# Kernel tuning notes

Measured on AMD Instinct MI355X. Metric: run time of the kernel, lower is better.

The kernel has to match this reference:

```python
import jax, jax.numpy as jnp
import numpy as np

B, T_DEC, T_ENC = 64, 128, 256
D_X, N_HIDDEN, N_FEED = 1024, 1024, 1024


def _glorot(key, shape):
    fan_in = shape[0]
    return jax.random.normal(key, shape, dtype=jnp.float32) / np.sqrt(fan_in)


def setup_inputs() -> dict:
    key = jax.random.key(0)
    ks = jax.random.split(key, 10)
    H = N_HIDDEN
    return {
        "x": jax.random.normal(ks[0], (B, T_DEC, D_X), dtype=jnp.float32),
        "o_enc": jax.random.normal(ks[1], (B, T_ENC, H), dtype=jnp.float32),
        "h_enc": jax.random.normal(ks[2], (B, H), dtype=jnp.float32),
        # input-feeding FFN: Dense(n_feed, tanh), input dim = n_hidden
        "Wfeed": _glorot(ks[3], (H, N_FEED)),
        "bfeed": jnp.zeros((N_FEED,), dtype=jnp.float32),
        # GRU (keras v2, reset_after=True): kernel [n_feed+d_x, 3H], recurrent [H, 3H]
        "Wx": _glorot(ks[4], (N_FEED + D_X, 3 * H)),
        "Wh": _glorot(ks[5], (H, 3 * H)),
        "bxi": jnp.zeros((3 * H,), dtype=jnp.float32),  # input bias
        "bhr": jnp.zeros((3 * H,), dtype=jnp.float32),  # recurrent bias (reset_after)
        # attention FFN: Dense(n_hidden, tanh), input dim = 2H (concat[value, h_dec])
        "Watt": _glorot(ks[6], (2 * H, H)),
        "batt": jnp.zeros((H,), dtype=jnp.float32),
    }


def reference(x, o_enc, h_enc, Wfeed, bfeed, Wx, Wh, bxi, bhr, Watt, batt):
    # x: [B, T_dec, d_x], o_enc: [B, T_enc, H], h_enc: [B, H]
    def step(carry, x_t):
        h, i_feed = carry  # h: [B,H] GRU state, i_feed: [B,H] previous attention output
        # input feeding FFN + concat with current token
        i_cat = jnp.concatenate([jnp.tanh(i_feed @ Wfeed + bfeed), x_t], axis=-1)
        # GRU cell (keras reset_after=True semantics)
        gx = i_cat @ Wx + bxi  # [B, 3H]
        gh = h @ Wh + bhr      # [B, 3H]
        xz, xr, xh = jnp.split(gx, 3, axis=-1)
        hz, hr, hh = jnp.split(gh, 3, axis=-1)
        z = jax.nn.sigmoid(xz + hz)
        r = jax.nn.sigmoid(xr + hr)
        hcand = jnp.tanh(xh + r * hh)
        h_new = z * h + (1.0 - z) * hcand  # [B, H]
        # Luong dot attention over encoder outputs
        scores = jnp.einsum('bh,bth->bt', h_new, o_enc)       # [B, T_enc]
        attn = jax.nn.softmax(scores, axis=-1)
        value = jnp.einsum('bt,bth->bh', attn, o_enc)         # [B, H]
        h_att = jnp.tanh(jnp.concatenate([value, h_new], axis=-1) @ Watt + batt)
        return (h_new, h_att), h_att

    i_feed0 = jnp.zeros_like(h_enc)
    x_t_major = jnp.swapaxes(x, 0, 1)  # [T_dec, B, d_x]
    _, outs = jax.lax.scan(step, (h_enc, i_feed0), x_t_major)
    return jnp.swapaxes(outs, 0, 1)  # [B, T_dec, H]
```

## Files before the change

kernel.cpp:

```cpp
#include <hip/hip_runtime.h>
#include <hip/hip_bf16.h>
#include <hip/hip_fp16.h>


#define NWG 256
#define NTHR 1024
constexpr int BB = 64, TD = 128, TE = 256, HH = 1024, H3 = 3072;
constexpr unsigned SMEM_BYTES = 155696;

typedef __attribute__((ext_vector_type(8))) __bf16 bf16x8;
typedef __attribute__((ext_vector_type(4))) float f32x4;
typedef __attribute__((ext_vector_type(4))) _Float16 f16x4;
using bf = __hip_bfloat16;
using hf = _Float16;

__device__ __forceinline__ f32x4 mfma16(bf16x8 a, bf16x8 b, f32x4 c) {
  return __builtin_amdgcn_mfma_f32_16x16x32_bf16(a, b, c, 0, 0, 0);
}

struct Args {
  const float *x, *bfeed, *bxi, *bhr, *batt;
  const hf *ohi, *olo;
  const bf *Wf0, *Wf1, *Wf2, *Wh0, *Wh1, *Wh2;
  const bf *WxF0, *WxF1, *WxF2, *WxX0, *WxX1, *WxX2, *Wa0, *Wa1, *Wa2;
  float *h_f32;
  float *gx;
  float *gh, *scores;
  bf *hs0, *hs1, *hs2, *ff0, *ff1, *ff2, *ifd0, *ifd1, *ifd2;
  bf *xt0, *xt1, *xt2, *vl0, *vl1, *vl2;
  unsigned *cnt, *cnt2, *go, *afl, *gox, *ffc, *ffx;
  float *out;
};

__device__ __forceinline__ void gbar(unsigned ep, const Args& a, int wg) {
  __syncthreads();
  if (threadIdx.x == 0) {
    __threadfence();
    unsigned* sub = a.cnt + (wg & 15) * 32;
    unsigned o = __hip_atomic_fetch_add(sub, 1u, __ATOMIC_ACQ_REL, __HIP_MEMORY_SCOPE_AGENT);
    if (o == 15) {
      __hip_atomic_store(sub, 0u, __ATOMIC_RELAXED, __HIP_MEMORY_SCOPE_AGENT);
      unsigned o2 = __hip_atomic_fetch_add(a.cnt2, 1u, __ATOMIC_ACQ_REL, __HIP_MEMORY_SCOPE_AGENT);
      if (o2 == 15) {
        __hip_atomic_store(a.cnt2, 0u, __ATOMIC_RELAXED, __HIP_MEMORY_SCOPE_AGENT);
        __hip_atomic_store(a.go, ep, __ATOMIC_RELEASE, __HIP_MEMORY_SCOPE_AGENT);
      }
    }
    if (wg < 8) {
      while (__hip_atomic_load(a.go, __ATOMIC_RELAXED, __HIP_MEMORY_SCOPE_AGENT) < ep)
        __builtin_amdgcn_s_sleep(1);
      __hip_atomic_store(a.gox + wg * 32, ep, __ATOMIC_RELEASE, __HIP_MEMORY_SCOPE_AGENT);
    } else {
      while (__hip_atomic_load(a.gox + (wg & 7) * 32, __ATOMIC_RELAXED,
                               __HIP_MEMORY_SCOPE_AGENT) < ep)
        __builtin_amdgcn_s_sleep(1);
    }
    __threadfence();
  }
  __syncthreads();
}

__device__ __forceinline__ void split3_write(bf* p0, bf* p1, bf* p2, size_t i, float v) {
  bf b0 = __float2bfloat16(v);
  float r1 = v - __bfloat162float(b0);
  bf b1 = __float2bfloat16(r1);
  float r2 = r1 - __bfloat162float(b1);
  p0[i] = b0; p1[i] = b1; p2[i] = __float2bfloat16(r2);
}

template <int K>
__device__ __forceinline__ f32x4 gemm6(const bf* A0, const bf* A1, const bf* A2,
                                       const bf* B0, const bf* B1, const bf* B2) {
  f32x4 c0 = {0.f, 0.f, 0.f, 0.f}, c1 = c0, c2 = c0, c3 = c0;
  bf16x8 a0 = *(const bf16x8*)(A0);
  bf16x8 a1 = *(const bf16x8*)(A1);
  bf16x8 a2 = *(const bf16x8*)(A2);
  bf16x8 b0 = *(const bf16x8*)(B0);
  bf16x8 b1 = *(const bf16x8*)(B1);
  bf16x8 b2 = *(const bf16x8*)(B2);
#pragma unroll
  for (int k = 0; k < K; k += 32) {
    bf16x8 na0, na1, na2, nb0, nb1, nb2;
    if (k + 32 < K) {
      na0 = *(const bf16x8*)(A0 + k + 32);
      na1 = *(const bf16x8*)(A1 + k + 32);
      na2 = *(const bf16x8*)(A2 + k + 32);
      nb0 = *(const bf16x8*)(B0 + k + 32);
      nb1 = *(const bf16x8*)(B1 + k + 32);
      nb2 = *(const bf16x8*)(B2 + k + 32);
    }
    c0 = mfma16(a0, b0, c0);
    c1 = mfma16(a0, b1, c1);
    c2 = mfma16(a1, b0, c2);
    c3 = mfma16(a1, b1, c3);
    c0 = mfma16(a0, b2, c0);
    c1 = mfma16(a2, b0, c1);
    if (k + 32 < K) {
      a0 = na0; a1 = na1; a2 = na2;
      b0 = nb0; b1 = nb1; b2 = nb2;
    }
  }
  f32x4 s;
#pragma unroll
  for (int i = 0; i < 4; ++i) s[i] = (c0[i] + c1[i]) + (c2[i] + c3[i]);
  return s;
}

__global__ __launch_bounds__(NTHR, 4) void decoder_main(Args a) {
  const int wg = blockIdx.x;
  const int tid = threadIdx.x;
  const int lane = tid & 63;
  const int wv = tid >> 6;
  const int lrow = lane & 15;
  const int lkg = lane >> 4;

  extern __shared__ char smem[];
  hf* o_hi     = (hf*)smem;
  float* s_u   = (float*)(smem + 131072);
  float* s_h   = (float*)(smem + 147456);
  float* s_sm  = (float*)(smem + 151552);
  float* s_val = (float*)(smem + 152576);
  int* s_idx   = (int*)(smem + 154624);
  int* s_wcnt  = (int*)(smem + 155648);
  float* s_red = (float*)(smem + 155664);

  const int b3 = wg & 63, q3 = wg >> 6;
  {
    const ushort* src = (const ushort*)(a.ohi + ((size_t)b3 * TE + q3 * 64) * HH);
    ushort* dst = (ushort*)o_hi;
#pragma unroll 4
    for (int i = tid; i < 16384; i += NTHR)
      ((ushort4*)dst)[i] = ((const ushort4*)src)[i];
  }

  unsigned ep = 0;

  for (int t = 0; t < TD; ++t) {
    {
      const bool isf = (wg < 64);
      const int j0 = (isf ? wg : wg - 64) * 16;
      const bf* A0 = isf ? a.ifd0 : a.hs0;
      const bf* A1 = isf ? a.ifd1 : a.hs1;
      const bf* A2 = isf ? a.ifd2 : a.hs2;
      const bf* B0 = isf ? a.Wf0 : a.Wh0;
      const bf* B1 = isf ? a.Wf1 : a.Wh1;
      const bf* B2 = isf ? a.Wf2 : a.Wh2;
      const int mt = wv >> 2, kq = wv & 3;
      const size_t aoff = (size_t)(mt * 16 + lrow) * HH + kq * 256 + lkg * 8;
      const size_t boff = (size_t)(j0 + lrow) * HH + kq * 256 + lkg * 8;
      f32x4 acc = gemm6<256>(A0 + aoff, A1 + aoff, A2 + aoff, B0 + boff, B1 + boff, B2 + boff);
#pragma unroll
      for (int r = 0; r < 4; ++r) s_u[kq * 1024 + mt * 256 + (lkg * 4 + r) * 16 + lrow] = acc[r];
      __syncthreads();
      {
        const int row = tid >> 4, c = tid & 15;
        const int emt = row >> 4, r2 = row & 15;
        const int e = emt * 256 + r2 * 16 + c;
        float v = (s_u[e] + s_u[1024 + e]) + (s_u[2048 + e] + s_u[3072 + e]);
        const int col = j0 + c;
        if (isf) {
          float f = tanhf(v + a.bfeed[col]);
          split3_write(a.ff0, a.ff1, a.ff2, (size_t)row * HH + col, f);
        } else {
          a.gh[(size_t)row * H3 + col] = v + a.bhr[col];
        }
      }
      __syncthreads();
      if (isf && tid == 0) {
        __threadfence();
        __hip_atomic_fetch_add(a.ffc, 1u, __ATOMIC_ACQ_REL, __HIP_MEMORY_SCOPE_AGENT);
      }
    }
    if (tid == 0) {
      const unsigned tgt = 64u * (unsigned)(t + 1);
      if (wg < 8) {
        while (__hip_atomic_load(a.ffc, __ATOMIC_RELAXED, __HIP_MEMORY_SCOPE_AGENT) < tgt)
          __builtin_amdgcn_s_sleep(1);
        __hip_atomic_store(a.ffx + wg * 32, tgt, __ATOMIC_RELEASE, __HIP_MEMORY_SCOPE_AGENT);
      } else {
        while (__hip_atomic_load(a.ffx + (wg & 7) * 32, __ATOMIC_RELAXED,
                                 __HIP_MEMORY_SCOPE_AGENT) < tgt)
          __builtin_amdgcn_s_sleep(1);
      }
      __threadfence();
    }
    __syncthreads();

    {
      const int xcd = wg & 7, slot = wg >> 3;
      const int jt = xcd * 8 + (slot >> 2), sub = slot & 3;
      if (wv < 12) {
        const int ci = wv >> 2, ku = wv & 3;
        const int c2 = sub * 3 + ci;
        const int g = c2 >> 2, mt = c2 & 3;
        const int op = ku >> 1, kh = ku & 1;
        const bf* A0 = op ? a.xt0 : a.ff0;
        const bf* A1 = op ? a.xt1 : a.ff1;
        const bf* A2 = op ? a.xt2 : a.ff2;
        const bf* B0 = op ? a.WxX0 : a.WxF0;
        const bf* B1 = op ? a.WxX1 : a.WxF1;
        const bf* B2 = op ? a.WxX2 : a.WxF2;
        const size_t aoff = (size_t)(mt * 16 + lrow) * HH + kh * 512 + lkg * 8;
        const size_t boff = (size_t)(g * HH + jt * 16 + lrow) * HH + kh * 512 + lkg * 8;
        f32x4 acc = gemm6<512>(A0 + aoff, A1 + aoff, A2 + aoff, B0 + boff, B1 + boff, B2 + boff);
#pragma unroll
        for (int r = 0; r < 4; ++r)
          s_u[ci * 1024 + ku * 256 + (lkg * 4 + r) * 16 + lrow] = acc[r];
      }
      __syncthreads();
      if (tid < 768) {
        const int ci2 = tid >> 8, e = tid & 255;
        const int r16 = e >> 4, c16 = e & 15;
        const int base = ci2 * 1024 + e;
        float v = (s_u[base] + s_u[base + 256]) + (s_u[base + 512] + s_u[base + 768]);
        const int c2 = sub * 3 + ci2;
        const int g = c2 >> 2, mt = c2 & 3;
        a.gx[(size_t)(mt * 16 + r16) * H3 + g * 1024 + jt * 16 + c16] = v;
      }
    }
    gbar(++ep, a, wg);

    {
      const int b = b3, q = q3;
      const float* hold = a.h_f32 + (size_t)(t & 1) * (BB * HH);
      float* hnew = a.h_f32 + (size_t)((t + 1) & 1) * (BB * HH);
      const float* ghb = a.gh + (size_t)b * H3;
      {
        const int col = tid;
        const float* gxb = a.gx + (size_t)b * H3;
        float gz = a.bxi[col] + gxb[col];
        float gr = a.bxi[HH + col] + gxb[HH + col];
        float gc = a.bxi[2 * HH + col] + gxb[2 * HH + col];
        float z = 1.f / (1.f + expf(-(gz + ghb[col])));
        float rr = 1.f / (1.f + expf(-(gr + ghb[HH + col])));
        float hc = tanhf(gc + rr * ghb[2 * HH + col]);
        float hn = z * hold[(size_t)b * HH + col] + (1.f - z) * hc;
        s_h[col] = hn;
        if (q == 0) {
          hnew[(size_t)b * HH + col] = hn;
          split3_write(a.hs0, a.hs1, a.hs2, (size_t)b * HH + col, hn);
        }
      }
      __syncthreads();
      {
        f32x4 sh0 = *(const f32x4*)(s_h + 0 + lane * 4);
        f32x4 sh1 = *(const f32x4*)(s_h + 256 + lane * 4);
        f32x4 sh2 = *(const f32x4*)(s_h + 512 + lane * 4);
        f32x4 sh3 = *(const f32x4*)(s_h + 768 + lane * 4);
        const hf* lobase = a.olo + ((size_t)b * TE + q * 64 + wv * 4) * HH + lane * 4;
        f16x4 l0 = *(const f16x4*)(lobase);
        f16x4 l1 = *(const f16x4*)(lobase + 256);
        f16x4 l2 = *(const f16x4*)(lobase + 512);
        f16x4 l3 = *(const f16x4*)(lobase + 768);
#pragma unroll
        for (int i = 0; i < 4; ++i) {
          f16x4 n0, n1, n2, n3;
          if (i + 1 < 4) {
            const hf* nr = lobase + (size_t)(i + 1) * HH;
            n0 = *(const f16x4*)(nr);
            n1 = *(const f16x4*)(nr + 256);
            n2 = *(const f16x4*)(nr + 512);
            n3 = *(const f16x4*)(nr + 768);
          }
          const hf* hrow = o_hi + (size_t)(wv * 4 + i) * HH + lane * 4;
          f16x4 h0 = *(const f16x4*)(hrow);
          f16x4 h1 = *(const f16x4*)(hrow + 256);
          f16x4 h2 = *(const f16x4*)(hrow + 512);
          f16x4 h3 = *(const f16x4*)(hrow + 768);
          float shi = (float)h0[0] * sh0[0] + (float)h0[1] * sh0[1] + (float)h0[2] * sh0[2] + (float)h0[3] * sh0[3]
                    + (float)h1[0] * sh1[0] + (float)h1[1] * sh1[1] + (float)h1[2] * sh1[2] + (float)h1[3] * sh1[3]
                    + (float)h2[0] * sh2[0] + (float)h2[1] * sh2[1] + (float)h2[2] * sh2[2] + (float)h2[3] * sh2[3]
                    + (float)h3[0] * sh3[0] + (float)h3[1] * sh3[1] + (float)h3[2] * sh3[2] + (float)h3[3] * sh3[3];
          float slo = (float)l0[0] * sh0[0] + (float)l0[1] * sh0[1] + (float)l0[2] * sh0[2] + (float)l0[3] * sh0[3]
                    + (float)l1[0] * sh1[0] + (float)l1[1] * sh1[1] + (float)l1[2] * sh1[2] + (float)l1[3] * sh1[3]
                    + (float)l2[0] * sh2[0] + (float)l2[1] * sh2[1] + (float)l2[2] * sh2[2] + (float)l2[3] * sh2[3]
                    + (float)l3[0] * sh3[0] + (float)l3[1] * sh3[1] + (float)l3[2] * sh3[2] + (float)l3[3] * sh3[3];
          float s = shi + slo * (1.0f / 2048.0f);
          for (int off = 32; off; off >>= 1) s += __shfl_xor(s, off);
          if (lane == 0) a.scores[(size_t)b * TE + q * 64 + wv * 4 + i] = s;
          l0 = n0; l1 = n1; l2 = n2; l3 = n3;
        }
      }
      __syncthreads();
      if (tid == 0) {
        __threadfence();
        __hip_atomic_store(&a.afl[b * 4 + q], (unsigned)(t + 1),
                           __ATOMIC_RELEASE, __HIP_MEMORY_SCOPE_AGENT);
        for (int p = 1; p < 4; ++p) {
          unsigned idx = b * 4 + ((q + p) & 3);
          while (__hip_atomic_load(&a.afl[idx], __ATOMIC_RELAXED, __HIP_MEMORY_SCOPE_AGENT)
                 < (unsigned)(t + 1))
            __builtin_amdgcn_s_sleep(1);
        }
        __threadfence();
      }
      __syncthreads();
      float sc = 0.f, p = 0.f;
      if (tid < 256) {
        sc = a.scores[(size_t)b * TE + tid];
        float v = sc;
        for (int off = 32; off; off >>= 1) v = fmaxf(v, __shfl_xor(v, off));
        if (lane == 0) s_red[wv] = v;
      }
      __syncthreads();
      {
        float mx = fmaxf(fmaxf(s_red[0], s_red[1]), fmaxf(s_red[2], s_red[3]));
        if (tid < 256) {
          p = expf(sc - mx);
          float sum = p;
          for (int off = 32; off; off >>= 1) sum += __shfl_xor(sum, off);
          if (lane == 0) s_red[4 + wv] = sum;
        }
      }
      __syncthreads();
      bool act = false;
      unsigned long long bm = 0;
      if (tid < 256) {
        float tot = s_red[4] + s_red[5] + s_red[6] + s_red[7];
        float w2 = p / tot;
        s_sm[tid] = w2;
        act = (w2 > 1e-8f);
        bm = __ballot(act);
        if (lane == 0) s_wcnt[wv] = __popcll(bm);
      }
      __syncthreads();
      if (tid < 256 && act) {
        int base = 0;
        for (int w2i = 0; w2i < wv; ++w2i) base += s_wcnt[w2i];
        int pos = base + __popcll(bm & ((1ULL << lane) - 1));
        s_idx[pos] = tid;
      }
      __syncthreads();
      const int nact = s_wcnt[0] + s_wcnt[1] + s_wcnt[2] + s_wcnt[3];
      if (tid < 512) {
        const int c = tid & 255, th = tid >> 8;
        const int j = q * 256 + c;
        const hf* hib = a.ohi + (size_t)b * TE * HH + j;
        const hf* lob = a.olo + (size_t)b * TE * HH + j;
        float accv = 0.f;
        int ii = th;
        for (; ii + 6 < nact; ii += 8) {
          const int i0 = s_idx[ii], i1 = s_idx[ii + 2], i2 = s_idx[ii + 4], i3 = s_idx[ii + 6];
          const float h0 = (float)hib[(size_t)i0 * HH], l0 = (float)lob[(size_t)i0 * HH];
          const float h1 = (float)hib[(size_t)i1 * HH], l1 = (float)lob[(size_t)i1 * HH];
          const float h2 = (float)hib[(size_t)i2 * HH], l2 = (float)lob[(size_t)i2 * HH];
          const float h3 = (float)hib[(size_t)i3 * HH], l3 = (float)lob[(size_t)i3 * HH];
          accv += s_sm[i0] * (h0 + l0 * (1.0f / 2048.0f));
          accv += s_sm[i1] * (h1 + l1 * (1.0f / 2048.0f));
          accv += s_sm[i2] * (h2 + l2 * (1.0f / 2048.0f));
          accv += s_sm[i3] * (h3 + l3 * (1.0f / 2048.0f));
        }
        for (; ii < nact; ii += 2) {
          const int tt2 = s_idx[ii];
          accv += s_sm[tt2] * ((float)hib[(size_t)tt2 * HH] +
                               (float)lob[(size_t)tt2 * HH] * (1.0f / 2048.0f));
        }
        s_val[th * 256 + c] = accv;
      }
      __syncthreads();
      if (tid < 256)
        split3_write(a.vl0, a.vl1, a.vl2, (size_t)b * HH + q * 256 + tid,
                     s_val[tid] + s_val[256 + tid]);
    }
    gbar(++ep, a, wg);

    {
      const int cu = wg & 63;
      const int mt = wg >> 6;
      const int kq16 = wv;
      const bool isv = (kq16 < 8);
      const int koff = (kq16 & 7) * 128;
      const bf* A0 = isv ? a.vl0 : a.hs0;
      const bf* A1 = isv ? a.vl1 : a.hs1;
      const bf* A2 = isv ? a.vl2 : a.hs2;
      const size_t aoff = (size_t)(mt * 16 + lrow) * HH + koff + lkg * 8;
      const size_t boff = (size_t)(cu * 16 + lrow) * 2048 + kq16 * 128 + lkg * 8;
      f32x4 acc = gemm6<128>(A0 + aoff, A1 + aoff, A2 + aoff,
                             a.Wa0 + boff, a.Wa1 + boff, a.Wa2 + boff);
#pragma unroll
      for (int r = 0; r < 4; ++r)
        s_u[kq16 * 256 + (lkg * 4 + r) * 16 + lrow] = acc[r];
      __syncthreads();
      if (tid < 256) {
        const int r16 = tid >> 4, c16 = tid & 15;
        const int e = r16 * 16 + c16;
        float v = a.batt[cu * 16 + c16];
#pragma unroll
        for (int kq = 0; kq < 16; ++kq) v += s_u[kq * 256 + e];
        float hv = tanhf(v);
        const int row = mt * 16 + r16;
        const int col = cu * 16 + c16;
        a.out[((size_t)row * TD + t) * HH + col] = hv;
        split3_write(a.ifd0, a.ifd1, a.ifd2, (size_t)row * HH + col, hv);
      }
      if (wg < 64 && t + 1 < TD) {
        split3_write(a.xt0, a.xt1, a.xt2, (size_t)wg * HH + tid,
                     a.x[((size_t)wg * TD + (t + 1)) * HH + tid]);
      }
    }
    gbar(++ep, a, wg);
  }
}

__global__ void k_tr3(const float* src, bf* d0, bf* d1, bf* d2, int R, int C) {
  __shared__ float tile[32][33];
  int c0 = blockIdx.x * 32, r0 = blockIdx.y * 32;
  int tx = threadIdx.x & 31, ty = threadIdx.x >> 5;
  for (int i = ty; i < 32; i += 8)
    tile[i][tx] = src[(size_t)(r0 + i) * C + c0 + tx];
  __syncthreads();
  for (int i = ty; i < 32; i += 8) {
    float v = tile[tx][i];
    size_t o = (size_t)(c0 + i) * R + r0 + tx;
    bf b0 = __float2bfloat16(v);
    float r1 = v - __bfloat162float(b0);
    bf b1 = __float2bfloat16(r1);
    d0[o] = b0; d1[o] = b1; d2[o] = __float2bfloat16(r1 - __bfloat162float(b1));
  }
}

__global__ void k_osplit(const float* src, hf* dhi, hf* dlo) {
  size_t i = (size_t)blockIdx.x * blockDim.x + threadIdx.x;
  float v = src[i];
  hf h = (hf)v;
  dhi[i] = h;
  dlo[i] = (hf)((v - (float)h) * 2048.0f);
}

__global__ void k_init(const float* h_enc, float* h_f32, bf* h0, bf* h1, bf* h2,
                       bf* i0, bf* i1, bf* i2, const float* x, bf* x0, bf* x1, bf* x2) {
  int i = blockIdx.x * blockDim.x + threadIdx.x;
  float v = h_enc[i];
  h_f32[i] = v;
  split3_write(h0, h1, h2, i, v);
  bf z = __float2bfloat16(0.f);
  i0[i] = z; i1[i] = z; i2[i] = z;
  int row = i >> 10, col = i & 1023;
  split3_write(x0, x1, x2, i, x[((size_t)row * TD + 0) * HH + col]);
}

extern "C" void kernel_launch(void* const* d_in, const int* in_sizes, int n_in,
                              void* d_out, int out_size, void* d_ws, size_t ws_size,
                              hipStream_t stream) {
  const float* x     = (const float*)d_in[0];
  const float* o_enc = (const float*)d_in[1];
  const float* h_enc = (const float*)d_in[2];
  const float* Wfeed = (const float*)d_in[3];
  const float* bfeed = (const float*)d_in[4];
  const float* Wx    = (const float*)d_in[5];
  const float* Wh    = (const float*)d_in[6];
  const float* bxi   = (const float*)d_in[7];
  const float* bhr   = (const float*)d_in[8];
  const float* Watt  = (const float*)d_in[9];
  const float* batt  = (const float*)d_in[10];

  char* w = (char*)d_ws;
  auto alloc = [&](size_t b) { char* p = w; w += (b + 255) & ~255ULL; return p; };

  const size_t M1 = (size_t)1024 * 1024 * 2;
  bf* Wf[3];  for (auto& p : Wf)  p = (bf*)alloc(M1);
  bf* Wh_[3]; for (auto& p : Wh_) p = (bf*)alloc(3 * M1);
  bf* WxF[3]; for (auto& p : WxF) p = (bf*)alloc(3 * M1);
  bf* WxX[3]; for (auto& p : WxX) p = (bf*)alloc(3 * M1);
  bf* Wa[3];  for (auto& p : Wa)  p = (bf*)alloc(2 * M1);
  hf* ohi = (hf*)alloc((size_t)BB * TE * HH * 2);
  hf* olo = (hf*)alloc((size_t)BB * TE * HH * 2);
  float* h_f32  = (float*)alloc((size_t)2 * BB * HH * 4);
  float* gx     = (float*)alloc((size_t)BB * H3 * 4);
  float* gh     = (float*)alloc((size_t)BB * H3 * 4);
  float* scores = (float*)alloc((size_t)BB * TE * 4);
  const size_t AB = (size_t)BB * HH * 2;
  bf *hs[3], *ff[3], *ifd[3], *xt[3], *vl[3];
  for (auto& p : hs)  p = (bf*)alloc(AB);
  for (auto& p : ff)  p = (bf*)alloc(AB);
  for (auto& p : ifd) p = (bf*)alloc(AB);
  for (auto& p : xt)  p = (bf*)alloc(AB);
  for (auto& p : vl)  p = (bf*)alloc(AB);
  unsigned* flags = (unsigned*)alloc(8192);

  hipMemsetAsync(flags, 0, 8192, stream);
  k_tr3<<<dim3(32, 32), 256, 0, stream>>>(Wfeed, Wf[0], Wf[1], Wf[2], 1024, 1024);
  k_tr3<<<dim3(96, 32), 256, 0, stream>>>(Wx, WxF[0], WxF[1], WxF[2], 1024, 3072);
  k_tr3<<<dim3(96, 32), 256, 0, stream>>>(Wx + (size_t)1024 * 3072, WxX[0], WxX[1], WxX[2], 1024, 3072);
  k_tr3<<<dim3(96, 32), 256, 0, stream>>>(Wh, Wh_[0], Wh_[1], Wh_[2], 1024, 3072);
  k_tr3<<<dim3(32, 64), 256, 0, stream>>>(Watt, Wa[0], Wa[1], Wa[2], 2048, 1024);
  k_osplit<<<(BB * TE * HH) / 256, 256, 0, stream>>>(o_enc, ohi, olo);
  k_init<<<BB * HH / 256, 256, 0, stream>>>(h_enc, h_f32, hs[0], hs[1], hs[2],
                                            ifd[0], ifd[1], ifd[2], x, xt[0], xt[1], xt[2]);

  Args a;
  a.x = x; a.bfeed = bfeed; a.bxi = bxi; a.bhr = bhr; a.batt = batt;
  a.ohi = ohi; a.olo = olo;
  a.Wf0 = Wf[0]; a.Wf1 = Wf[1]; a.Wf2 = Wf[2];
  a.Wh0 = Wh_[0]; a.Wh1 = Wh_[1]; a.Wh2 = Wh_[2];
  a.WxF0 = WxF[0]; a.WxF1 = WxF[1]; a.WxF2 = WxF[2];
  a.WxX0 = WxX[0]; a.WxX1 = WxX[1]; a.WxX2 = WxX[2];
  a.Wa0 = Wa[0]; a.Wa1 = Wa[1]; a.Wa2 = Wa[2];
  a.h_f32 = h_f32; a.gx = gx; a.gh = gh; a.scores = scores;
  a.hs0 = hs[0]; a.hs1 = hs[1]; a.hs2 = hs[2];
  a.ff0 = ff[0]; a.ff1 = ff[1]; a.ff2 = ff[2];
  a.ifd0 = ifd[0]; a.ifd1 = ifd[1]; a.ifd2 = ifd[2];
  a.xt0 = xt[0]; a.xt1 = xt[1]; a.xt2 = xt[2];
  a.vl0 = vl[0]; a.vl1 = vl[1]; a.vl2 = vl[2];
  a.cnt = flags; a.cnt2 = flags + 512; a.go = flags + 544; a.afl = flags + 576;
  a.gox = flags + 832; a.ffc = flags + 1088; a.ffx = flags + 1120;
  a.out = (float*)d_out;

  hipFuncSetAttribute((const void*)decoder_main,
                      hipFuncAttributeMaxDynamicSharedMemorySize, SMEM_BYTES);
  decoder_main<<<NWG, NTHR, SMEM_BYTES, stream>>>(a);
}
```

Measured before the change: 20.95 ms.

## Compute attention value locally per quarter with split softmax and deeper GEMM prefetch

Each workgroup now keeps its own 64 encoder rows' scores in shared memory and computes a local max and sum. Quartets exchange these through global memory so the softmax can be normalised without writing and rereading the full score vector. Each workgroup then computes a partial attention value over all 1024 columns from its own smem-resident hi half, and the four partials are combined after a second quartet sync. The gemm6 inner loop also prefetches three K-steps ahead instead of one. The cost is an extra cross-workgroup sync, more global traffic for the partial-value buffer, and more registers in gemm6.

Result: slower. 22.66 ms (+8.1%).

```diff
diff --git a/kernel.cpp b/kernel.cpp
--- a/kernel.cpp
+++ b/kernel.cpp
@@ -6,7 +6,7 @@
 #define NWG 256
 #define NTHR 1024
 constexpr int BB = 64, TD = 128, TE = 256, HH = 1024, H3 = 3072;
-constexpr unsigned SMEM_BYTES = 155696;
+constexpr unsigned SMEM_BYTES = 152576;
 
 typedef __attribute__((ext_vector_type(8))) __bf16 bf16x8;
 typedef __attribute__((ext_vector_type(4))) float f32x4;
@@ -25,10 +25,12 @@
   const bf *WxF0, *WxF1, *WxF2, *WxX0, *WxX1, *WxX2, *Wa0, *Wa1, *Wa2;
   float *h_f32;
   float *gx;
-  float *gh, *scores;
+  float *gh;
+  float *mS;
+  float *vpart;
   bf *hs0, *hs1, *hs2, *ff0, *ff1, *ff2, *ifd0, *ifd1, *ifd2;
   bf *xt0, *xt1, *xt2, *vl0, *vl1, *vl2;
-  unsigned *cnt, *cnt2, *go, *afl, *gox, *ffc, *ffx;
+  unsigned *cnt, *cnt2, *go, *gox, *ffc, *ffx, *afl1, *afl2;
   float *out;
 };
 
@@ -60,6 +62,17 @@
   __syncthreads();
 }
 
+__device__ __forceinline__ void quartet_sync(unsigned* fl, int b, int q, unsigned tgt) {
+  __threadfence();
+  __hip_atomic_store(&fl[b * 4 + q], tgt, __ATOMIC_RELEASE, __HIP_MEMORY_SCOPE_AGENT);
+  for (int p = 1; p < 4; ++p) {
+    unsigned idx = b * 4 + ((q + p) & 3);
+    while (__hip_atomic_load(&fl[idx], __ATOMIC_RELAXED, __HIP_MEMORY_SCOPE_AGENT) < tgt)
+      __builtin_amdgcn_s_sleep(1);
+  }
+  __threadfence();
+}
+
 __device__ __forceinline__ void split3_write(bf* p0, bf* p1, bf* p2, size_t i, float v) {
   bf b0 = __float2bfloat16(v);
   float r1 = v - __bfloat162float(b0);
@@ -78,16 +91,28 @@
   bf16x8 b0 = *(const bf16x8*)(B0);
   bf16x8 b1 = *(const bf16x8*)(B1);
   bf16x8 b2 = *(const bf16x8*)(B2);
+  bf16x8 xa0 = *(const bf16x8*)(A0 + 32);
+  bf16x8 xa1 = *(const bf16x8*)(A1 + 32);
+  bf16x8 xa2 = *(const bf16x8*)(A2 + 32);
+  bf16x8 xb0 = *(const bf16x8*)(B0 + 32);
+  bf16x8 xb1 = *(const bf16x8*)(B1 + 32);
+  bf16x8 xb2 = *(const bf16x8*)(B2 + 32);
+  bf16x8 ya0 = *(const bf16x8*)(A0 + 64);
+  bf16x8 ya1 = *(const bf16x8*)(A1 + 64);
+  bf16x8 ya2 = *(const bf16x8*)(A2 + 64);
+  bf16x8 yb0 = *(const bf16x8*)(B0 + 64);
+  bf16x8 yb1 = *(const bf16x8*)(B1 + 64);
+  bf16x8 yb2 = *(const bf16x8*)(B2 + 64);
 #pragma unroll
   for (int k = 0; k < K; k += 32) {
-    bf16x8 na0, na1, na2, nb0, nb1, nb2;
-    if (k + 32 < K) {
-      na0 = *(const bf16x8*)(A0 + k + 32);
-      na1 = *(const bf16x8*)(A1 + k + 32);
-      na2 = *(const bf16x8*)(A2 + k + 32);
-      nb0 = *(const bf16x8*)(B0 + k + 32);
-      nb1 = *(const bf16x8*)(B1 + k + 32);
-      nb2 = *(const bf16x8*)(B2 + k + 32);
+    bf16x8 n0, n1, n2, n3, n4, n5;
+    if (k + 96 < K) {
+      n0 = *(const bf16x8*)(A0 + k + 96);
+      n1 = *(const bf16x8*)(A1 + k + 96);
+      n2 = *(const bf16x8*)(A2 + k + 96);
+      n3 = *(const bf16x8*)(B0 + k + 96);
+      n4 = *(const bf16x8*)(B1 + k + 96);
+      n5 = *(const bf16x8*)(B2 + k + 96);
     }
     c0 = mfma16(a0, b0, c0);
     c1 = mfma16(a0, b1, c1);
@@ -95,9 +120,10 @@
     c3 = mfma16(a1, b1, c3);
     c0 = mfma16(a0, b2, c0);
     c1 = mfma16(a2, b0, c1);
-    if (k + 32 < K) {
-      a0 = na0; a1 = na1; a2 = na2;
-      b0 = nb0; b1 = nb1; b2 = nb2;
+    a0 = xa0; a1 = xa1; a2 = xa2; b0 = xb0; b1 = xb1; b2 = xb2;
+    xa0 = ya0; xa1 = ya1; xa2 = ya2; xb0 = yb0; xb1 = yb1; xb2 = yb2;
+    if (k + 96 < K) {
+      ya0 = n0; ya1 = n1; ya2 = n2; yb0 = n3; yb1 = n4; yb2 = n5;
     }
   }
   f32x4 s;
@@ -119,10 +145,6 @@
   float* s_u   = (float*)(smem + 131072);
   float* s_h   = (float*)(smem + 147456);
   float* s_sm  = (float*)(smem + 151552);
-  float* s_val = (float*)(smem + 152576);
-  int* s_idx   = (int*)(smem + 154624);
-  int* s_wcnt  = (int*)(smem + 155648);
-  float* s_red = (float*)(smem + 155664);
 
   const int b3 = wg & 63, q3 = wg >> 6;
   {
@@ -277,90 +299,61 @@
                     + (float)l3[0] * sh3[0] + (float)l3[1] * sh3[1] + (float)l3[2] * sh3[2] + (float)l3[3] * sh3[3];
           float s = shi + slo * (1.0f / 2048.0f);
           for (int off = 32; off; off >>= 1) s += __shfl_xor(s, off);
-          if (lane == 0) a.scores[(size_t)b * TE + q * 64 + wv * 4 + i] = s;
+          if (lane == 0) s_sm[wv * 4 + i] = s;
           l0 = n0; l1 = n1; l2 = n2; l3 = n3;
         }
       }
       __syncthreads();
-      if (tid == 0) {
-        __threadfence();
-        __hip_atomic_store(&a.afl[b * 4 + q], (unsigned)(t + 1),
-                           __ATOMIC_RELEASE, __HIP_MEMORY_SCOPE_AGENT);
-        for (int p = 1; p < 4; ++p) {
-          unsigned idx = b * 4 + ((q + p) & 3);
-          while (__hip_atomic_load(&a.afl[idx], __ATOMIC_RELAXED, __HIP_MEMORY_SCOPE_AGENT)
-                 < (unsigned)(t + 1))
-            __builtin_amdgcn_s_sleep(1);
+      if (tid < 64) {
+        float v = s_sm[tid];
+        float m = v;
+        for (int off = 32; off; off >>= 1) m = fmaxf(m, __shfl_xor(m, off));
+        float e2 = expf(v - m);
+        float S = e2;
+        for (int off = 32; off; off >>= 1) S += __shfl_xor(S, off);
+        if (tid == 0) {
+          a.mS[(b * 4 + q) * 2]     = m;
+          a.mS[(b * 4 + q) * 2 + 1] = S;
         }
-        __threadfence();
-      }
-      __syncthreads();
-      float sc = 0.f, p = 0.f;
+      }
+      __syncthreads();
+      if (tid == 0) quartet_sync(a.afl1, b, q, (unsigned)(t + 1));
+      __syncthreads();
+      if (tid < 64) {
+        float m0 = a.mS[(b * 4 + 0) * 2], S0 = a.mS[(b * 4 + 0) * 2 + 1];
+        float m1 = a.mS[(b * 4 + 1) * 2], S1 = a.mS[(b * 4 + 1) * 2 + 1];
+        float m2 = a.mS[(b * 4 + 2) * 2], S2 = a.mS[(b * 4 + 2) * 2 + 1];
+        float m3 = a.mS[(b * 4 + 3) * 2], S3 = a.mS[(b * 4 + 3) * 2 + 1];
+        float M = fmaxf(fmaxf(m0, m1), fmaxf(m2, m3));
+        float den = S0 * expf(m0 - M) + S1 * expf(m1 - M) +
+                    S2 * expf(m2 - M) + S3 * expf(m3 - M);
+        s_sm[tid] = expf(s_sm[tid] - M) / den;
+      }
+      __syncthreads();
+      {
+        float accv = 0.f;
+        const hf* lob = a.olo + ((size_t)b * TE + q * 64) * HH + tid;
+        for (int r = 0; r < 64; ++r) {
+          float w = s_sm[r];
+          if (w > 1e-8f) {
+            float hi = (float)o_hi[(size_t)r * HH + tid];
+            float lo = (float)lob[(size_t)r * HH];
+            accv += w * (hi + lo * (1.0f / 2048.0f));
+          }
+        }
+        a.vpart[(size_t)(b * 4 + q) * HH + tid] = accv;
+      }
+      __syncthreads();
+      if (tid == 0) quartet_sync(a.afl2, b, q, (unsigned)(t + 1));
+      __syncthreads();
       if (tid < 256) {
-        sc = a.scores[(size_t)b * TE + tid];
-        float v = sc;
-        for (int off = 32; off; off >>= 1) v = fmaxf(v, __shfl_xor(v, off));
-        if (lane == 0) s_red[wv] = v;
-      }
-      __syncthreads();
-      {
-        float mx = fmaxf(fmaxf(s_red[0], s_red[1]), fmaxf(s_red[2], s_red[3]));
-        if (tid < 256) {
-          p = expf(sc - mx);
-          float sum = p;
-          for (int off = 32; off; off >>= 1) sum += __shfl_xor(sum, off);
-          if (lane == 0) s_red[4 + wv] = sum;
-        }
-      }
-      __syncthreads();
-      bool act = false;
-      unsigned long long bm = 0;
-      if (tid < 256) {
-        float tot = s_red[4] + s_red[5] + s_red[6] + s_red[7];
-        float w2 = p / tot;
-        s_sm[tid] = w2;
-        act = (w2 > 1e-8f);
-        bm = __ballot(act);
-        if (lane == 0) s_wcnt[wv] = __popcll(bm);
-      }
-      __syncthreads();
-      if (tid < 256 && act) {
-        int base = 0;
-        for (int w2i = 0; w2i < wv; ++w2i) base += s_wcnt[w2i];
-        int pos = base + __popcll(bm & ((1ULL << lane) - 1));
-        s_idx[pos] = tid;
-      }
-      __syncthreads();
-      const int nact = s_wcnt[0] + s_wcnt[1] + s_wcnt[2] + s_wcnt[3];
-      if (tid < 512) {
-        const int c = tid & 255, th = tid >> 8;
-        const int j = q * 256 + c;
-        const hf* hib = a.ohi + (size_t)b * TE * HH + j;
-        const hf* lob = a.olo + (size_t)b * TE * HH + j;
-        float accv = 0.f;
-        int ii = th;
-        for (; ii + 6 < nact; ii += 8) {
-          const int i0 = s_idx[ii], i1 = s_idx[ii + 2], i2 = s_idx[ii + 4], i3 = s_idx[ii + 6];
-          const float h0 = (float)hib[(size_t)i0 * HH], l0 = (float)lob[(size_t)i0 * HH];
-          const float h1 = (float)hib[(size_t)i1 * HH], l1 = (float)lob[(size_t)i1 * HH];
-          const float h2 = (float)hib[(size_t)i2 * HH], l2 = (float)lob[(size_t)i2 * HH];
-          const float h3 = (float)hib[(size_t)i3 * HH], l3 = (float)lob[(size_t)i3 * HH];
-          accv += s_sm[i0] * (h0 + l0 * (1.0f / 2048.0f));
-          accv += s_sm[i1] * (h1 + l1 * (1.0f / 2048.0f));
-          accv += s_sm[i2] * (h2 + l2 * (1.0f / 2048.0f));
-          accv += s_sm[i3] * (h3 + l3 * (1.0f / 2048.0f));
-        }
-        for (; ii < nact; ii += 2) {
-          const int tt2 = s_idx[ii];
-          accv += s_sm[tt2] * ((float)hib[(size_t)tt2 * HH] +
-                               (float)lob[(size_t)tt2 * HH] * (1.0f / 2048.0f));
-        }
-        s_val[th * 256 + c] = accv;
-      }
-      __syncthreads();
-      if (tid < 256)
-        split3_write(a.vl0, a.vl1, a.vl2, (size_t)b * HH + q * 256 + tid,
-                     s_val[tid] + s_val[256 + tid]);
+        const int col = q * 256 + tid;
+        float v = (a.vpart[(size_t)(b * 4 + 0) * HH + col] +
+                   a.vpart[(size_t)(b * 4 + 1) * HH + col]) +
+                  (a.vpart[(size_t)(b * 4 + 2) * HH + col] +
+                   a.vpart[(size_t)(b * 4 + 3) * HH + col]);
+        split3_write(a.vl0, a.vl1, a.vl2, (size_t)b * HH + col, v);
+      }
     }
     gbar(++ep, a, wg);
 
@@ -465,10 +458,11 @@
   bf* Wa[3];  for (auto& p : Wa)  p = (bf*)alloc(2 * M1);
   hf* ohi = (hf*)alloc((size_t)BB * TE * HH * 2);
   hf* olo = (hf*)alloc((size_t)BB * TE * HH * 2);
-  float* h_f32  = (float*)alloc((size_t)2 * BB * HH * 4);
-  float* gx     = (float*)alloc((size_t)BB * H3 * 4);
-  float* gh     = (float*)alloc((size_t)BB * H3 * 4);
-  float* scores = (float*)alloc((size_t)BB * TE * 4);
+  float* h_f32 = (float*)alloc((size_t)2 * BB * HH * 4);
+  float* gx    = (float*)alloc((size_t)BB * H3 * 4);
+  float* gh    = (float*)alloc((size_t)BB * H3 * 4);
+  float* mS    = (float*)alloc(256 * 2 * 4);
+  float* vpart = (float*)alloc((size_t)256 * HH * 4);
   const size_t AB = (size_t)BB * HH * 2;
   bf *hs[3], *ff[3], *ifd[3], *xt[3], *vl[3];
   for (auto& p : hs)  p = (bf*)alloc(AB);
@@ -476,9 +470,9 @@
   for (auto& p : ifd) p = (bf*)alloc(AB);
   for (auto& p : xt)  p = (bf*)alloc(AB);
   for (auto& p : vl)  p = (bf*)alloc(AB);
-  unsigned* flags = (unsigned*)alloc(8192);
-
-  hipMemsetAsync(flags, 0, 8192, stream);
+  unsigned* flags = (unsigned*)alloc(16384);
+
+  hipMemsetAsync(flags, 0, 16384, stream);
   k_tr3<<<dim3(32, 32), 256, 0, stream>>>(Wfeed, Wf[0], Wf[1], Wf[2], 1024, 1024);
   k_tr3<<<dim3(96, 32), 256, 0, stream>>>(Wx, WxF[0], WxF[1], WxF[2], 1024, 3072);
   k_tr3<<<dim3(96, 32), 256, 0, stream>>>(Wx + (size_t)1024 * 3072, WxX[0], WxX[1], WxX[2], 1024, 3072);
@@ -496,14 +490,20 @@
   a.WxF0 = WxF[0]; a.WxF1 = WxF[1]; a.WxF2 = WxF[2];
   a.WxX0 = WxX[0]; a.WxX1 = WxX[1]; a.WxX2 = WxX[2];
   a.Wa0 = Wa[0]; a.Wa1 = Wa[1]; a.Wa2 = Wa[2];
-  a.h_f32 = h_f32; a.gx = gx; a.gh = gh; a.scores = scores;
+  a.h_f32 = h_f32; a.gx = gx; a.gh = gh; a.mS = mS; a.vpart = vpart;
   a.hs0 = hs[0]; a.hs1 = hs[1]; a.hs2 = hs[2];
   a.ff0 = ff[0]; a.ff1 = ff[1]; a.ff2 = ff[2];
   a.ifd0 = ifd[0]; a.ifd1 = ifd[1]; a.ifd2 = ifd[2];
   a.xt0 = xt[0]; a.xt1 = xt[1]; a.xt2 = xt[2];
   a.vl0 = vl[0]; a.vl1 = vl[1]; a.vl2 = vl[2];
-  a.cnt = flags; a.cnt2 = flags + 512; a.go = flags + 544; a.afl = flags + 576;
-  a.gox = flags + 832; a.ffc = flags + 1088; a.ffx = flags + 1120;
+  a.cnt = flags;
+  a.cnt2 = flags + 512;
+  a.go = flags + 544;
+  a.gox = flags + 576;
+  a.ffc = flags + 832;
+  a.ffx = flags + 864;
+  a.afl1 = flags + 1152;
+  a.afl2 = flags + 1408;
   a.out = (float*)d_out;
 
   hipFuncSetAttribute((const void*)decoder_main,
```
